# Performance work log

Measured on AMD Instinct MI355X. Metric: run time of the kernel, lower is better.

Reference implementation:

```python
import jax, jax.numpy as jnp
import numpy as np

B, S, D = 4, 4096, 1024
P = int(D * 1.333)  # 1364, matches torch int(d_model * proj_factor)
CAP = 15.0
EPS = 1e-6


def _rmsnorm(x, w, eps=EPS):
    xf = x.astype(jnp.float32)
    var = jnp.mean(xf * xf, axis=-1, keepdims=True)
    return w * (xf * jax.lax.rsqrt(var + eps)).astype(x.dtype)


def _softcap_sigmoid(g):
    # sigmoid(cap * tanh(g / cap))
    return jax.nn.sigmoid(CAP * jnp.tanh(g / CAP))


def setup_inputs() -> dict:
    key = jax.random.key(0)
    k0, k1, k2, k3 = jax.random.split(key, 4)
    x = jax.random.normal(k0, (B, S, D), jnp.float32)
    hidden_state = jnp.zeros((B, P), jnp.float32)
    ln_weight = jnp.ones((D,), jnp.float32)
    W_gate = jax.random.normal(k1, (D, 3 * P), jnp.float32) / np.sqrt(D).astype(np.float32)
    W_cell = jax.random.normal(k2, (D, P), jnp.float32) / np.sqrt(D).astype(np.float32)
    W_out = jax.random.normal(k3, (P, D), jnp.float32) / np.sqrt(P).astype(np.float32)
    return {"x": x, "hidden_state": hidden_state, "ln_weight": ln_weight,
            "W_gate": W_gate, "W_cell": W_cell, "W_out": W_out}


def reference(x, hidden_state, ln_weight, W_gate, W_cell, W_out):
    b, s, d = x.shape
    residual = x
    xn = _rmsnorm(x, ln_weight)
    # gate projection -> [b, s, 3, P], unbind gate types
    gates = jnp.einsum('bsd,dk->bsk', xn, W_gate).reshape(b, s, 3, P)
    i_gate = _softcap_sigmoid(gates[:, :, 0])
    f_gate = _softcap_sigmoid(gates[:, :, 1])
    o_gate = _softcap_sigmoid(gates[:, :, 2])
    c_input = jnp.einsum('bsd,dp->bsp', xn, W_cell)

    # sequential linear recurrence: h_t = f_t * h_{t-1} + i_t * tanh(c_t)
    def step(h, inp):
        c_t, i_t, f_t, o_t = inp
        h = f_t * h + i_t * jnp.tanh(c_t)
        return h, o_t * jnp.tanh(h)

    seq = (jnp.swapaxes(c_input, 0, 1), jnp.swapaxes(i_gate, 0, 1),
           jnp.swapaxes(f_gate, 0, 1), jnp.swapaxes(o_gate, 0, 1))  # time-major [s,b,P]
    _, outs = jax.lax.scan(step, hidden_state, seq)
    outputs = jnp.swapaxes(outs, 0, 1)  # [b, s, P]

    out = residual + jnp.einsum('bsp,pd->bsd', outputs, W_out)
    # NOTE: original torch module returns the UNMODIFIED initial hidden_state
    return out, hidden_state
```

## Files before the change

### kernel.cpp

```cpp
#include <hip/hip_runtime.h>
#include <hip/hip_bf16.h>
#include <math.h>
#include <stdint.h>

typedef __bf16 bf16_t;
typedef bf16_t bf16x2 __attribute__((ext_vector_type(2)));
typedef bf16_t bf16x4 __attribute__((ext_vector_type(4)));
typedef bf16_t bf16x8 __attribute__((ext_vector_type(8)));
typedef float floatx4 __attribute__((ext_vector_type(4)));

#define B_     4
#define S_     4096
#define D_     1024
#define P_     1364
#define P3_    4092
#define NP_    5456
#define NPAD_  5504
#define NB_    5632
#define KPAD_  1408
#define ROWS_  16384
#define CAP_   15.0f
#define EPS_   1e-6f
#define CHUNKS_ 32
#define CLEN_   128

__device__ __forceinline__ float fast_tanh(float x) {
    x = fminf(fmaxf(x, -15.f), 15.f);
    float e = __expf(2.f * x);
    return __fdividef(e - 1.f, e + 1.f);
}
__device__ __forceinline__ float fast_sig(float g) {
    return __fdividef(1.f, 1.f + __expf(-g));
}

__device__ __forceinline__ void vmcnt0() {
    asm volatile("s_waitcnt vmcnt(0)" ::: "memory");
}
__device__ __forceinline__ void vmcnt8() {
    asm volatile("s_waitcnt vmcnt(8)" ::: "memory");
}

__global__ __launch_bounds__(256) void rmsnorm_kernel(const float* __restrict__ x,
                                                      const float* __restrict__ w,
                                                      bf16_t* __restrict__ xn) {
    int row = blockIdx.x;
    int tid = threadIdx.x;
    const float4 v = ((const float4*)(x + (size_t)row * D_))[tid];
    float ss = v.x * v.x + v.y * v.y + v.z * v.z + v.w * v.w;
    #pragma unroll
    for (int off = 32; off > 0; off >>= 1) ss += __shfl_down(ss, off);
    __shared__ float red[4];
    if ((tid & 63) == 0) red[tid >> 6] = ss;
    __syncthreads();
    float tot = red[0] + red[1] + red[2] + red[3];
    float scale = rsqrtf(tot * (1.0f / (float)D_) + EPS_);
    const float4 wv = ((const float4*)w)[tid];
    bf16x4 o;
    o[0] = (bf16_t)(v.x * scale * wv.x);
    o[1] = (bf16_t)(v.y * scale * wv.y);
    o[2] = (bf16_t)(v.z * scale * wv.z);
    o[3] = (bf16_t)(v.w * scale * wv.w);
    ((bf16x4*)(xn + (size_t)row * D_))[tid] = o;
}

__global__ __launch_bounds__(256) void pack_wcat(const float* __restrict__ Wg,
                                                 const float* __restrict__ Wc,
                                                 bf16_t* __restrict__ Wt) {
    __shared__ float tile[32][33];
    int kt = blockIdx.x * 32;
    int nt = blockIdx.y * 32;
    int tx = threadIdx.x & 31;
    int ty = threadIdx.x >> 5;
    #pragma unroll
    for (int i = 0; i < 4; i++) {
        int k = kt + ty + 8 * i;
        int n = nt + tx;
        float val = 0.f;
        if (n < P3_)      val = Wg[(size_t)k * P3_ + n];
        else if (n < NP_) val = Wc[(size_t)k * P_ + (n - P3_)];
        tile[ty + 8 * i][tx] = val;
    }
    __syncthreads();
    #pragma unroll
    for (int i = 0; i < 4; i++) {
        int n = nt + ty + 8 * i;
        int k = kt + tx;
        Wt[(size_t)n * D_ + k] = (bf16_t)tile[tx][ty + 8 * i];
    }
}

__global__ __launch_bounds__(256) void pack_wout(const float* __restrict__ Wo,
                                                 bf16_t* __restrict__ Wt) {
    __shared__ float tile[32][33];
    int pt = blockIdx.x * 32;
    int dt = blockIdx.y * 32;
    int tx = threadIdx.x & 31;
    int ty = threadIdx.x >> 5;
    #pragma unroll
    for (int i = 0; i < 4; i++) {
        int p = pt + ty + 8 * i;
        int d = dt + tx;
        float val = (p < P_) ? Wo[(size_t)p * D_ + d] : 0.f;
        tile[ty + 8 * i][tx] = val;
    }
    __syncthreads();
    #pragma unroll
    for (int i = 0; i < 4; i++) {
        int d = dt + ty + 8 * i;
        int p = pt + tx;
        Wt[(size_t)d * KPAD_ + p] = (bf16_t)tile[tx][ty + 8 * i];
    }
}

template <int KTOT, int LDA, int LDB, int LDC, int NX, int EPI>
__global__ __launch_bounds__(512, 2) void gemm8(const bf16_t* __restrict__ A,
                                                const bf16_t* __restrict__ Bt,
                                                const float* __restrict__ res,
                                                void* __restrict__ outv) {
    constexpr int NT = KTOT / 64;
    static_assert(NT >= 4, "NT >= 4");
    __shared__ __align__(16) char smem[131072];

    const int tid  = threadIdx.x;
    const int wid  = tid >> 6;
    const int lane = tid & 63;
    const int l15  = lane & 15;
    const int sl4  = lane >> 4;
    const int sp    = sl4 ^ ((lane >> 1) & 3);
    const int chunk = (lane & 3) ^ ((lane >> 3) & 3);
    const int wrow = (wid >> 2) * 128;
    const int wcol = (wid & 3) * 64;

    constexpr int MCH = (ROWS_ / 256) / 8;
    const int bid = blockIdx.x;
    const int xcd = bid & 7;
    const int idx = bid >> 3;
    const int bx  = idx / MCH;
    const int by  = xcd * MCH + (idx - bx * MCH);
    const int m0 = by * 256, n0 = bx * 256;

    const int srow = wid * 16 + (lane >> 2);
    const bf16_t* Asrc = A  + (size_t)(m0 + srow) * LDA + chunk * 8;
    const bf16_t* Bsrc = Bt + (size_t)(n0 + srow) * LDB + chunk * 8;
    const unsigned ldsA0 = (unsigned)(wid * 1024);
    const unsigned ldsB0 = 32768u + (unsigned)(wid * 1024);

    auto stageAlo = [&](int kt, int buf) {
        #pragma unroll
        for (int kk = 0; kk < 2; kk++)
            __builtin_amdgcn_global_load_lds(
                (const unsigned*)(Asrc + kt * 64 + kk * 32),
                (unsigned*)(smem + ((unsigned)buf * 65536u + (unsigned)kk * 16384u + ldsA0)), 16, 0, 0);
    };
    auto stageAhi = [&](int kt, int buf) {
        #pragma unroll
        for (int kk = 0; kk < 2; kk++)
            __builtin_amdgcn_global_load_lds(
                (const unsigned*)(Asrc + (size_t)128 * LDA + kt * 64 + kk * 32),
                (unsigned*)(smem + ((unsigned)buf * 65536u + (unsigned)kk * 16384u + 8192u + ldsA0)), 16, 0, 0);
    };
    auto stageBlo = [&](int kt, int buf) {
        #pragma unroll
        for (int kk = 0; kk < 2; kk++)
            __builtin_amdgcn_global_load_lds(
                (const unsigned*)(Bsrc + kt * 64 + kk * 32),
                (unsigned*)(smem + ((unsigned)buf * 65536u + (unsigned)kk * 16384u + ldsB0)), 16, 0, 0);
    };
    auto stageBhi = [&](int kt, int buf) {
        #pragma unroll
        for (int kk = 0; kk < 2; kk++)
            __builtin_amdgcn_global_load_lds(
                (const unsigned*)(Bsrc + (size_t)128 * LDB + kt * 64 + kk * 32),
                (unsigned*)(smem + ((unsigned)buf * 65536u + (unsigned)kk * 16384u + 8192u + ldsB0)), 16, 0, 0);
    };
    auto ldA = [&](int buf, int kk, int m) -> bf16x8 {
        return *(const bf16x8*)(smem + (buf * 65536 + kk * 16384 +
                                        (wrow + m * 16 + l15) * 64 + sp * 16));
    };
    auto ldB = [&](int buf, int kk, int n) -> bf16x8 {
        return *(const bf16x8*)(smem + (buf * 65536 + 32768 + kk * 16384 +
                                        (wcol + n * 16 + l15) * 64 + sp * 16));
    };

    floatx4 acc[8][4];
    #pragma unroll
    for (int m = 0; m < 8; m++)
        #pragma unroll
        for (int n = 0; n < 4; n++) acc[m][n] = (floatx4){0.f, 0.f, 0.f, 0.f};

    bf16x8 aq[8];
    bf16x8 bq[4];
    bf16x8 bq2[4];

    stageAlo(0, 0); stageAhi(0, 0); stageBlo(0, 0); stageBhi(0, 0);
    stageAlo(1, 1); stageAhi(1, 1); stageBlo(1, 1); stageBhi(1, 1);
    vmcnt8();
    __builtin_amdgcn_s_barrier();

    for (int t = 0; t < NT; ++t) {
        const int c = t & 1;
        const bool st = (t + 2 < NT);

        #pragma unroll
        for (int m = 0; m < 4; m++) { aq[m] = ldA(c, 0, m); aq[m + 4] = ldA(c, 1, m); }
        #pragma unroll
        for (int n = 0; n < 2; n++) { bq[n] = ldB(c, 0, n); bq[n + 2] = ldB(c, 1, n); }
        __builtin_amdgcn_s_barrier();
        __builtin_amdgcn_s_setprio(1);
        #pragma unroll
        for (int m = 0; m < 4; m++)
            #pragma unroll
            for (int n = 0; n < 2; n++) {
                acc[m][n] = __builtin_amdgcn_mfma_f32_16x16x32_bf16(bq[n], aq[m], acc[m][n], 0, 0, 0);
                acc[m][n] = __builtin_amdgcn_mfma_f32_16x16x32_bf16(bq[n + 2], aq[m + 4], acc[m][n], 0, 0, 0);
            }
        __builtin_amdgcn_s_setprio(0);
        __builtin_amdgcn_s_barrier();

        #pragma unroll
        for (int n = 0; n < 2; n++) { bq2[n] = ldB(c, 0, n + 2); bq2[n + 2] = ldB(c, 1, n + 2); }
        if (st) stageBlo(t + 2, c);
        __builtin_amdgcn_s_barrier();
        __builtin_amdgcn_s_setprio(1);
        #pragma unroll
        for (int m = 0; m < 4; m++)
            #pragma unroll
            for (int n = 0; n < 2; n++) {
                acc[m][n + 2] = __builtin_amdgcn_mfma_f32_16x16x32_bf16(bq2[n], aq[m], acc[m][n + 2], 0, 0, 0);
                acc[m][n + 2] = __builtin_amdgcn_mfma_f32_16x16x32_bf16(bq2[n + 2], aq[m + 4], acc[m][n + 2], 0, 0, 0);
            }
        __builtin_amdgcn_s_setprio(0);
        __builtin_amdgcn_s_barrier();

        #pragma unroll
        for (int m = 0; m < 4; m++) { aq[m] = ldA(c, 0, m + 4); aq[m + 4] = ldA(c, 1, m + 4); }
        if (st) stageAlo(t + 2, c);
        __builtin_amdgcn_s_barrier();
        __builtin_amdgcn_s_setprio(1);
        #pragma unroll
        for (int m = 0; m < 4; m++)
            #pragma unroll
            for (int n = 0; n < 2; n++) {
                acc[m + 4][n + 2] = __builtin_amdgcn_mfma_f32_16x16x32_bf16(bq2[n], aq[m], acc[m + 4][n + 2], 0, 0, 0);
                acc[m + 4][n + 2] = __builtin_amdgcn_mfma_f32_16x16x32_bf16(bq2[n + 2], aq[m + 4], acc[m + 4][n + 2], 0, 0, 0);
            }
        __builtin_amdgcn_s_setprio(0);
        __builtin_amdgcn_s_barrier();

        if (st) { stageAhi(t + 2, c); stageBhi(t + 2, c); }
        __builtin_amdgcn_s_setprio(1);
        #pragma unroll
        for (int m = 0; m < 4; m++)
            #pragma unroll
            for (int n = 0; n < 2; n++) {
                acc[m + 4][n] = __builtin_amdgcn_mfma_f32_16x16x32_bf16(bq[n], aq[m], acc[m + 4][n], 0, 0, 0);
                acc[m + 4][n] = __builtin_amdgcn_mfma_f32_16x16x32_bf16(bq[n + 2], aq[m + 4], acc[m + 4][n], 0, 0, 0);
            }
        __builtin_amdgcn_s_setprio(0);
        if (st)                vmcnt8();
        else if (t + 2 == NT)  vmcnt0();
        __builtin_amdgcn_s_barrier();
    }

    if constexpr (EPI == 0) {
        bf16_t* O = (bf16_t*)outv;
        #pragma unroll
        for (int m = 0; m < 8; m++) {
            const int row = m0 + wrow + m * 16 + l15;
            #pragma unroll
            for (int n = 0; n < 4; n++) {
                const int cb = n0 + wcol + n * 16 + sl4 * 4;
                if (cb < NP_) {
                    const bool sg = cb < P3_;
                    bf16x4 o;
                    #pragma unroll
                    for (int r = 0; r < 4; r++) {
                        float g = acc[m][n][r];
                        o[r] = (bf16_t)(sg ? fast_sig(g) : fast_tanh(g));
                    }
                    *(bf16x4*)(O + (size_t)row * LDC + cb) = o;
                }
            }
        }
    } else {
        float* O = (float*)outv;
        #pragma unroll
        for (int m = 0; m < 8; m++) {
            const int row = m0 + wrow + m * 16 + l15;
            #pragma unroll
            for (int n = 0; n < 4; n++) {
                const int cb = n0 + wcol + n * 16 + sl4 * 4;
                const float4 rv = *(const float4*)(res + (size_t)row * LDC + cb);
                float4 ov;
                ov.x = rv.x + acc[m][n][0];
                ov.y = rv.y + acc[m][n][1];
                ov.z = rv.z + acc[m][n][2];
                ov.w = rv.w + acc[m][n][3];
                *(float4*)(O + (size_t)row * LDC + cb) = ov;
            }
        }
    }
}

__global__ __launch_bounds__(256) void chunk_scan1(const bf16_t* __restrict__ act,
                                                   float* __restrict__ FA) {
    int p = blockIdx.x * 256 + threadIdx.x;
    int c = blockIdx.y;
    int b = blockIdx.z;
    if (p >= P_) return;
    const bf16_t* base = act + (size_t)(b * S_ + c * CLEN_) * NPAD_;
    float F = 1.f, Acc = 0.f;
    for (int t = 0; t < CLEN_; t++) {
        const bf16_t* r = base + (size_t)t * NPAD_;
        float iv = (float)r[p];
        float fv = (float)r[P_ + p];
        float tc = (float)r[P3_ + p];
        Acc = fv * Acc + iv * tc;
        F *= fv;
    }
    size_t idx = (((size_t)b * CHUNKS_ + c) * P_ + p) * 2;
    FA[idx]     = F;
    FA[idx + 1] = Acc;
}

__global__ __launch_bounds__(256) void chunk_scan2(const bf16_t* __restrict__ act,
                                                   const float* __restrict__ FA,
                                                   const float* __restrict__ h0,
                                                   bf16_t* __restrict__ outp) {
    int p = blockIdx.x * 256 + threadIdx.x;
    int c = blockIdx.y;
    int b = blockIdx.z;
    if (p >= KPAD_) return;
    if (p >= P_) {
        bf16_t z = (bf16_t)0.f;
        for (int t = 0; t < CLEN_; t++)
            outp[(size_t)(b * S_ + c * CLEN_ + t) * KPAD_ + p] = z;
        return;
    }
    float h = h0[(size_t)b * P_ + p];
    for (int j = 0; j < c; j++) {
        size_t idx = (((size_t)b * CHUNKS_ + j) * P_ + p) * 2;
        h = FA[idx + 1] + FA[idx] * h;
    }
    const bf16_t* base = act + (size_t)(b * S_ + c * CLEN_) * NPAD_;
    bf16_t* ob = outp + (size_t)(b * S_ + c * CLEN_) * KPAD_;
    for (int t = 0; t < CLEN_; t++) {
        const bf16_t* r = base + (size_t)t * NPAD_;
        float iv = (float)r[p];
        float fv = (float)r[P_ + p];
        float ov = (float)r[2 * P_ + p];
        float tc = (float)r[P3_ + p];
        h = fv * h + iv * tc;
        ob[(size_t)t * KPAD_ + p] = (bf16_t)(ov * fast_tanh(h));
    }
}

__global__ void copy_hidden(const float* __restrict__ hs, float* __restrict__ dst) {
    int i = blockIdx.x * 256 + threadIdx.x;
    if (i < B_ * P_) dst[i] = hs[i];
}

extern "C" void kernel_launch(void* const* d_in, const int* in_sizes, int n_in,
                              void* d_out, int out_size, void* d_ws, size_t ws_size,
                              hipStream_t stream) {
    const float* x   = (const float*)d_in[0];
    const float* hs  = (const float*)d_in[1];
    const float* lnw = (const float*)d_in[2];
    const float* Wg  = (const float*)d_in[3];
    const float* Wc  = (const float*)d_in[4];
    const float* Wo  = (const float*)d_in[5];
    float* out = (float*)d_out;

    char* ws = (char*)d_ws;
    size_t off = 0;
    auto alloc = [&](size_t bytes) {
        void* p = ws + off;
        off += (bytes + 255) & ~(size_t)255;
        return p;
    };
    bf16_t* xn_outp = (bf16_t*)alloc((size_t)ROWS_ * KPAD_ * 2);
    bf16_t* act     = (bf16_t*)alloc((size_t)ROWS_ * NPAD_ * 2);
    bf16_t* WcatT   = (bf16_t*)alloc((size_t)NB_ * D_ * 2);
    bf16_t* WoutT   = (bf16_t*)alloc((size_t)D_ * KPAD_ * 2);
    float*  FA      = (float*)alloc((size_t)B_ * CHUNKS_ * P_ * 2 * 4);

    bf16_t* xn   = xn_outp;
    bf16_t* outp = xn_outp;

    hipLaunchKernelGGL(rmsnorm_kernel, dim3(ROWS_), dim3(256), 0, stream, x, lnw, xn);
    hipLaunchKernelGGL(pack_wcat, dim3(32, NB_ / 32), dim3(256), 0, stream, Wg, Wc, WcatT);
    hipLaunchKernelGGL(pack_wout, dim3(KPAD_ / 32, D_ / 32), dim3(256), 0, stream, Wo, WoutT);

    hipLaunchKernelGGL((gemm8<D_, D_, D_, NPAD_, NB_ / 256, 0>),
                       dim3((NB_ / 256) * (ROWS_ / 256)), dim3(512), 0, stream,
                       xn, WcatT, (const float*)nullptr, (void*)act);

    hipLaunchKernelGGL(chunk_scan1, dim3(6, CHUNKS_, B_), dim3(256), 0, stream, act, FA);
    hipLaunchKernelGGL(chunk_scan2, dim3(6, CHUNKS_, B_), dim3(256), 0, stream, act, FA, hs, outp);

    hipLaunchKernelGGL((gemm8<KPAD_, KPAD_, KPAD_, D_, D_ / 256, 1>),
                       dim3((D_ / 256) * (ROWS_ / 256)), dim3(512), 0, stream,
                       outp, WoutT, x, d_out);

    hipLaunchKernelGGL(copy_hidden, dim3((B_ * P_ + 255) / 256), dim3(256), 0, stream,
                       hs, out + (size_t)ROWS_ * D_);
}
```

Baseline: 426.1 us.

## Drop intra-iteration GEMM barriers and vectorize chunk scans to two channels per thread

Removes three s_barrier calls between the LDS fragment loads and the MFMA blocks in the GEMM main loop, so there is less warp synchronisation. Separately, the two chunked-scan kernels now process two adjacent channels per thread with bf16x2 loads and float4 FA accesses, which halves the grid. Dropping the barriers risks LDS races, because staging writes for tile t+2 can now overlap other warps' reads of the current buffer. The scan changes cut the number of load instructions but also halve the thread-level parallelism in an already small launch.

```diff
diff --git a/kernel.cpp b/kernel.cpp
--- a/kernel.cpp
+++ b/kernel.cpp
@@ -205,7 +205,6 @@
         for (int m = 0; m < 4; m++) { aq[m] = ldA(c, 0, m); aq[m + 4] = ldA(c, 1, m); }
         #pragma unroll
         for (int n = 0; n < 2; n++) { bq[n] = ldB(c, 0, n); bq[n + 2] = ldB(c, 1, n); }
-        __builtin_amdgcn_s_barrier();
         __builtin_amdgcn_s_setprio(1);
         #pragma unroll
         for (int m = 0; m < 4; m++)
@@ -220,7 +219,6 @@
         #pragma unroll
         for (int n = 0; n < 2; n++) { bq2[n] = ldB(c, 0, n + 2); bq2[n + 2] = ldB(c, 1, n + 2); }
         if (st) stageBlo(t + 2, c);
-        __builtin_amdgcn_s_barrier();
         __builtin_amdgcn_s_setprio(1);
         #pragma unroll
         for (int m = 0; m < 4; m++)
@@ -235,7 +233,6 @@
         #pragma unroll
         for (int m = 0; m < 4; m++) { aq[m] = ldA(c, 0, m + 4); aq[m + 4] = ldA(c, 1, m + 4); }
         if (st) stageAlo(t + 2, c);
-        __builtin_amdgcn_s_barrier();
         __builtin_amdgcn_s_setprio(1);
         #pragma unroll
         for (int m = 0; m < 4; m++)
@@ -304,54 +301,61 @@
 
 __global__ __launch_bounds__(256) void chunk_scan1(const bf16_t* __restrict__ act,
                                                    float* __restrict__ FA) {
-    int p = blockIdx.x * 256 + threadIdx.x;
+    int p = (blockIdx.x * 256 + threadIdx.x) * 2;
     int c = blockIdx.y;
     int b = blockIdx.z;
     if (p >= P_) return;
     const bf16_t* base = act + (size_t)(b * S_ + c * CLEN_) * NPAD_;
-    float F = 1.f, Acc = 0.f;
+    float F0 = 1.f, F1 = 1.f, A0 = 0.f, A1 = 0.f;
     for (int t = 0; t < CLEN_; t++) {
         const bf16_t* r = base + (size_t)t * NPAD_;
-        float iv = (float)r[p];
-        float fv = (float)r[P_ + p];
-        float tc = (float)r[P3_ + p];
-        Acc = fv * Acc + iv * tc;
-        F *= fv;
-    }
-    size_t idx = (((size_t)b * CHUNKS_ + c) * P_ + p) * 2;
-    FA[idx]     = F;
-    FA[idx + 1] = Acc;
+        bf16x2 iv = *(const bf16x2*)(r + p);
+        bf16x2 fv = *(const bf16x2*)(r + P_ + p);
+        bf16x2 tc = *(const bf16x2*)(r + P3_ + p);
+        float f0 = (float)fv[0], f1 = (float)fv[1];
+        A0 = f0 * A0 + (float)iv[0] * (float)tc[0];
+        A1 = f1 * A1 + (float)iv[1] * (float)tc[1];
+        F0 *= f0; F1 *= f1;
+    }
+    float4 o; o.x = F0; o.y = A0; o.z = F1; o.w = A1;
+    *(float4*)(FA + (((size_t)b * CHUNKS_ + c) * P_ + p) * 2) = o;
 }
 
 __global__ __launch_bounds__(256) void chunk_scan2(const bf16_t* __restrict__ act,
                                                    const float* __restrict__ FA,
                                                    const float* __restrict__ h0,
                                                    bf16_t* __restrict__ outp) {
-    int p = blockIdx.x * 256 + threadIdx.x;
+    int p = (blockIdx.x * 256 + threadIdx.x) * 2;
     int c = blockIdx.y;
     int b = blockIdx.z;
     if (p >= KPAD_) return;
+    bf16_t* ob = outp + (size_t)(b * S_ + c * CLEN_) * KPAD_;
     if (p >= P_) {
-        bf16_t z = (bf16_t)0.f;
+        bf16x2 z; z[0] = (bf16_t)0.f; z[1] = (bf16_t)0.f;
         for (int t = 0; t < CLEN_; t++)
-            outp[(size_t)(b * S_ + c * CLEN_ + t) * KPAD_ + p] = z;
+            *(bf16x2*)(ob + (size_t)t * KPAD_ + p) = z;
         return;
     }
-    float h = h0[(size_t)b * P_ + p];
+    float h0v = h0[(size_t)b * P_ + p];
+    float h1v = h0[(size_t)b * P_ + p + 1];
     for (int j = 0; j < c; j++) {
-        size_t idx = (((size_t)b * CHUNKS_ + j) * P_ + p) * 2;
-        h = FA[idx + 1] + FA[idx] * h;
+        float4 fa = *(const float4*)(FA + (((size_t)b * CHUNKS_ + j) * P_ + p) * 2);
+        h0v = fa.y + fa.x * h0v;
+        h1v = fa.w + fa.z * h1v;
     }
     const bf16_t* base = act + (size_t)(b * S_ + c * CLEN_) * NPAD_;
-    bf16_t* ob = outp + (size_t)(b * S_ + c * CLEN_) * KPAD_;
     for (int t = 0; t < CLEN_; t++) {
         const bf16_t* r = base + (size_t)t * NPAD_;
-        float iv = (float)r[p];
-        float fv = (float)r[P_ + p];
-        float ov = (float)r[2 * P_ + p];
-        float tc = (float)r[P3_ + p];
-        h = fv * h + iv * tc;
-        ob[(size_t)t * KPAD_ + p] = (bf16_t)(ov * fast_tanh(h));
+        bf16x2 iv = *(const bf16x2*)(r + p);
+        bf16x2 fv = *(const bf16x2*)(r + P_ + p);
+        bf16x2 ov = *(const bf16x2*)(r + 2 * P_ + p);
+        bf16x2 tc = *(const bf16x2*)(r + P3_ + p);
+        h0v = (float)fv[0] * h0v + (float)iv[0] * (float)tc[0];
+        h1v = (float)fv[1] * h1v + (float)iv[1] * (float)tc[1];
+        bf16x2 o;
+        o[0] = (bf16_t)((float)ov[0] * fast_tanh(h0v));
+        o[1] = (bf16_t)((float)ov[1] * fast_tanh(h1v));
+        *(bf16x2*)(ob + (size_t)t * KPAD_ + p) = o;
     }
 }
 
@@ -395,8 +399,8 @@
                        dim3((NB_ / 256) * (ROWS_ / 256)), dim3(512), 0, stream,
                        xn, WcatT, (const float*)nullptr, (void*)act);
 
-    hipLaunchKernelGGL(chunk_scan1, dim3(6, CHUNKS_, B_), dim3(256), 0, stream, act, FA);
-    hipLaunchKernelGGL(chunk_scan2, dim3(6, CHUNKS_, B_), dim3(256), 0, stream, act, FA, hs, outp);
+    hipLaunchKernelGGL(chunk_scan1, dim3(3, CHUNKS_, B_), dim3(256), 0, stream, act, FA);
+    hipLaunchKernelGGL(chunk_scan2, dim3(3, CHUNKS_, B_), dim3(256), 0, stream, act, FA, hs, outp);
 
     hipLaunchKernelGGL((gemm8<KPAD_, KPAD_, KPAD_, D_, D_ / 256, 1>),
                        dim3((D_ / 256) * (ROWS_ / 256)), dim3(512), 0, stream,
```

After: 444.1 us. 4.2% more time.
